# Kernel optimization log

Measured on AMD Instinct MI355X. Metric: run time of the kernel, lower is better.

Reference implementation:

```python
import jax, jax.numpy as jnp
import numpy as np

DIM = 768
HEADS = 12
HEAD_DIM = DIM // HEADS
ROPE_BASE = 100.0  # Dust3R uses freq=100 for its rotary embedding


def apply_rope(x):
    # x: [B, H, N, D] -> rotary embedding over token index (rotate-half form)
    B, H, N, D = x.shape
    pos = jnp.arange(N, dtype=jnp.float32)
    inv_freq = 1.0 / (ROPE_BASE ** (jnp.arange(0, D, 2, dtype=jnp.float32) / D))
    ang = pos[:, None] * inv_freq[None, :]            # [N, D/2]
    cos = jnp.concatenate([jnp.cos(ang), jnp.cos(ang)], axis=-1).astype(x.dtype)  # [N, D]
    sin = jnp.concatenate([jnp.sin(ang), jnp.sin(ang)], axis=-1).astype(x.dtype)
    x1, x2 = jnp.split(x, 2, axis=-1)
    x_rot = jnp.concatenate([-x2, x1], axis=-1)
    return x * cos + x_rot * sin


def setup_inputs() -> dict:
    key = jax.random.key(0)
    ks = jax.random.split(key, 8)
    B, N = 8, 1024
    scale = 0.02
    return {
        "query": jax.random.normal(ks[0], (B, N, DIM), jnp.float32),
        "key": jax.random.normal(ks[1], (B, N, DIM), jnp.float32),
        "value": jax.random.normal(ks[2], (B, N, DIM), jnp.float32),
        "Wq": jax.random.normal(ks[3], (DIM, DIM), jnp.float32) * scale,
        "Wk": jax.random.normal(ks[4], (DIM, DIM), jnp.float32) * scale,
        "Wv": jax.random.normal(ks[5], (DIM, DIM), jnp.float32) * scale,
        "Wo": jax.random.normal(ks[6], (DIM, DIM), jnp.float32) * scale,
        "bo": jax.random.normal(ks[7], (DIM,), jnp.float32) * scale,
    }


def reference(query, key, value, Wq, Wk, Wv, Wo, bo):
    B, Nq, C = query.shape
    H, D = HEADS, HEAD_DIM
    sm_scale = D ** -0.5
    # Linear projections (torch Linear: x @ W.T), split heads -> [B, H, N, D]
    q = jnp.einsum('bnc,dc->bnd', query, Wq).reshape(B, Nq, H, D).transpose(0, 2, 1, 3)
    k = jnp.einsum('bnc,dc->bnd', key, Wk).reshape(B, -1, H, D).transpose(0, 2, 1, 3)
    v = jnp.einsum('bnc,dc->bnd', value, Wv).reshape(B, -1, H, D).transpose(0, 2, 1, 3)
    q = apply_rope(q)
    k = apply_rope(k)
    attn = jnp.einsum('bhqd,bhkd->bhqk', q, k) * sm_scale
    attn = jax.nn.softmax(attn, axis=-1)
    x = jnp.einsum('bhqk,bhkd->bhqd', attn, v)
    x = x.transpose(0, 2, 1, 3).reshape(B, Nq, C)
    return jnp.einsum('bnc,dc->bnd', x, Wo) + bo
```

## Files before the change

kernel.cpp:

```cpp
#include <hip/hip_runtime.h>
#include <cmath>

typedef __bf16 bf16x8 __attribute__((ext_vector_type(8)));
typedef float f32x4 __attribute__((ext_vector_type(4)));
typedef unsigned short u16;

#define MFMA_BF16 __builtin_amdgcn_mfma_f32_16x16x32_bf16

__device__ __forceinline__ u16 f2bf(float f) {
  unsigned int u = __float_as_uint(f);
  u = (u + 0x7fffu + ((u >> 16) & 1u)) >> 16;
  return (u16)u;
}

__device__ __forceinline__ unsigned cvtpk(float lo, float hi) {
  unsigned r;
  asm("v_cvt_pk_bf16_f32 %0, %1, %2" : "=v"(r) : "v"(lo), "v"(hi));
  return r;
}

__device__ __forceinline__ void async16(const u16* g, u16* l) {
  __builtin_amdgcn_global_load_lds(
      (__attribute__((address_space(1))) void*)g,
      (__attribute__((address_space(3))) void*)l, 16, 0, 0);
}

__global__ __launch_bounds__(256) void cvt_bf16(const float4* __restrict__ in,
                                                uint2* __restrict__ out, int n4) {
  int i = blockIdx.x * 256 + threadIdx.x;
  if (i >= n4) return;
  float4 f = in[i];
  uint2 o;
  o.x = (unsigned)f2bf(f.x) | ((unsigned)f2bf(f.y) << 16);
  o.y = (unsigned)f2bf(f.z) | ((unsigned)f2bf(f.w) << 16);
  out[i] = o;
}

__global__ __launch_bounds__(256) void cvt_all(
    const float4* s0, const float4* s1, const float4* s2, const float4* s3,
    const float4* s4, const float4* s5, const float4* s6,
    uint2* d0, uint2* d1, uint2* d2, uint2* d3, uint2* d4, uint2* d5, uint2* d6) {
  int i = blockIdx.x * 256 + threadIdx.x;
  const float4* src;
  uint2* dst;
  int off;
  if (i < 1572864)      { src = s0; dst = d0; off = i; }
  else if (i < 3145728) { src = s1; dst = d1; off = i - 1572864; }
  else if (i < 4718592) { src = s2; dst = d2; off = i - 3145728; }
  else {
    int j = i - 4718592;
    int w = j / 147456;
    off = j - w * 147456;
    src = (w == 0) ? s3 : (w == 1) ? s4 : (w == 2) ? s5 : s6;
    dst = (w == 0) ? d3 : (w == 1) ? d4 : (w == 2) ? d5 : d6;
  }
  float4 f = src[off];
  uint2 o;
  o.x = (unsigned)f2bf(f.x) | ((unsigned)f2bf(f.y) << 16);
  o.y = (unsigned)f2bf(f.z) | ((unsigned)f2bf(f.w) << 16);
  dst[off] = o;
}

__device__ __forceinline__ void gemm_body(const u16* __restrict__ Ag,
                                          const u16* __restrict__ Wg,
                                          void* __restrict__ OutP,
                                          const float* __restrict__ bias,
                                          int mode, int bx, int by) {
  __shared__ alignas(16) u16 As[128][64];
  __shared__ alignas(16) u16 Bs[128][64];
  const int tid  = threadIdx.x;
  const int lane = tid & 63, wv = tid >> 6;
  const int l15  = lane & 15, quad = lane >> 4;
  const int row0 = bx * 128, col0 = by * 128;
  const int wr = (wv >> 1) * 64, wc = (wv & 1) * 64;
  const int swA = l15 & 7;

  size_t aSrc[4], bSrc[4];
  int dsts[4];
#pragma unroll
  for (int rr = 0; rr < 4; ++rr) {
    int c = rr * 256 + tid;
    int row = c >> 3, cp = c & 7;
    int gc = cp ^ (row & 7);
    aSrc[rr] = (size_t)(row0 + row) * 768 + gc * 8;
    bSrc[rr] = (size_t)(col0 + row) * 768 + gc * 8;
    dsts[rr] = c * 8;
  }

  f32x4 acc[4][4];
#pragma unroll
  for (int i = 0; i < 4; ++i)
#pragma unroll
    for (int j = 0; j < 4; ++j) acc[i][j] = (f32x4){0.f, 0.f, 0.f, 0.f};

  for (int kb = 0; kb < 768; kb += 64) {
#pragma unroll
    for (int rr = 0; rr < 4; ++rr) {
      async16(&Ag[aSrc[rr] + kb], &((u16*)As)[dsts[rr]]);
      async16(&Wg[bSrc[rr] + kb], &((u16*)Bs)[dsts[rr]]);
    }
    __syncthreads();
#pragma unroll
    for (int kd = 0; kd < 2; ++kd) {
      int cpk = ((kd * 4 + quad) ^ swA) * 8;
      bf16x8 af[4], bfr[4];
#pragma unroll
      for (int mt = 0; mt < 4; ++mt) af[mt] = *(const bf16x8*)&As[wr + mt * 16 + l15][cpk];
#pragma unroll
      for (int nt = 0; nt < 4; ++nt) bfr[nt] = *(const bf16x8*)&Bs[wc + nt * 16 + l15][cpk];
#pragma unroll
      for (int mt = 0; mt < 4; ++mt)
#pragma unroll
        for (int nt = 0; nt < 4; ++nt)
          acc[mt][nt] = MFMA_BF16(af[mt], bfr[nt], acc[mt][nt], 0, 0, 0);
    }
    __syncthreads();
  }

  if (mode == 3) {
    float* O = (float*)OutP;
#pragma unroll
    for (int mt = 0; mt < 4; ++mt)
#pragma unroll
      for (int r = 0; r < 4; ++r) {
        int m = row0 + wr + mt * 16 + quad * 4 + r;
#pragma unroll
        for (int nt = 0; nt < 4; ++nt) {
          int c = col0 + wc + nt * 16 + l15;
          O[(size_t)m * 768 + c] = acc[mt][nt][r] + bias[c];
        }
      }
  } else if (mode == 2) {
    u16* O = (u16*)OutP;
#pragma unroll
    for (int mt = 0; mt < 4; ++mt)
#pragma unroll
      for (int r = 0; r < 4; ++r) {
        int m = row0 + wr + mt * 16 + quad * 4 + r;
        int b = m >> 10, n = m & 1023;
#pragma unroll
        for (int nt = 0; nt < 4; ++nt) {
          int c = col0 + wc + nt * 16 + l15;
          O[(size_t)(b * 768 + c) * 1024 + n] = f2bf(acc[mt][nt][r]);
        }
      }
  } else {
    u16* O = (u16*)OutP;
    const float scale = (mode == 0) ? 0.125f * 1.44269504088896f : 1.0f;
    const float invf0 = exp2f(-6.6438561897747395f * (float)l15 * (1.0f / 32.0f));
    const float invf1 = exp2f(-6.6438561897747395f * (float)(16 + l15) * (1.0f / 32.0f));
#pragma unroll
    for (int mt = 0; mt < 4; ++mt)
#pragma unroll
      for (int r = 0; r < 4; ++r) {
        int m = row0 + wr + mt * 16 + quad * 4 + r;
        int b = m >> 10, n = m & 1023;
        float fn = (float)n;
        size_t rowbase = (size_t)b * 786432 + (size_t)n * 64;
#pragma unroll
        for (int nt = 0; nt < 2; ++nt) {
          float sv, cv;
          __sincosf(fn * (nt ? invf1 : invf0), &sv, &cv);
          float x1 = acc[mt][nt][r], x2 = acc[mt][nt + 2][r];
          int c1 = col0 + wc + nt * 16 + l15;
          int c2 = c1 + 32;
          O[rowbase + (size_t)(c1 >> 6) * 65536 + (c1 & 63)] = f2bf((x1 * cv - x2 * sv) * scale);
          O[rowbase + (size_t)(c2 >> 6) * 65536 + (c2 & 63)] = f2bf((x2 * cv + x1 * sv) * scale);
        }
      }
  }
}

__global__ __launch_bounds__(256, 3) void gemm768(const u16* __restrict__ A,
                                                  const u16* __restrict__ W,
                                                  void* __restrict__ OutP,
                                                  const float* __restrict__ bias,
                                                  int mode) {
  gemm_body(A, W, OutP, bias, mode, blockIdx.x, blockIdx.y);
}

__global__ __launch_bounds__(256, 3) void gemm_qkv(
    const u16* __restrict__ xq, const u16* __restrict__ xk, const u16* __restrict__ xv,
    const u16* __restrict__ wq, const u16* __restrict__ wk, const u16* __restrict__ wv,
    u16* __restrict__ qb, u16* __restrict__ kb, u16* __restrict__ vtb) {
  int z = blockIdx.z;
  const u16* A = (z == 0) ? xq : (z == 1) ? xk : xv;
  const u16* W = (z == 0) ? wq : (z == 1) ? wk : wv;
  void* O      = (z == 0) ? (void*)qb : (z == 1) ? (void*)kb : (void*)vtb;
  gemm_body(A, W, O, nullptr, z, blockIdx.x, blockIdx.y);
}

__global__ __launch_bounds__(256, 3) void attn_fused(const u16* __restrict__ Q,
                                                     const u16* __restrict__ K,
                                                     const u16* __restrict__ Vt,
                                                     u16* __restrict__ X) {
  __shared__ alignas(16) u16 KsF[2][4096];
  __shared__ alignas(16) u16 VsF[2][4096];
  __shared__ alignas(16) u16 Ps[4][2048];

  const int tid  = threadIdx.x;
  const int lane = tid & 63, wv = tid >> 6;
  const int l15  = lane & 15, quad = lane >> 4;
  const int bh = blockIdx.x, qt = blockIdx.y;
  const size_t base = (size_t)bh * 65536;
  const int sw8 = (quad ^ ((l15 >> 1) & 3)) * 8;
  const int swP = l15 & 7;

  const u16* Qg = Q + base + (size_t)qt * 8192;
  const u16* Kb = K + base;
  const u16* Vb = Vt + base;

  int kOff[2], vOff[2], dOff[2];
#pragma unroll
  for (int rr = 0; rr < 2; ++rr) {
    int c = rr * 256 + tid;
    int sub = c >> 8, rowi = (c >> 2) & 63, colc = c & 3;
    int cs = (colc ^ ((rowi >> 1) & 3)) * 8;
    kOff[rr] = rowi * 64 + sub * 32 + cs;
    vOff[rr] = rowi * 1024 + sub * 32 + cs;
    dOff[rr] = c * 8;
  }

  auto stageKV = [&](int kt, int bf) {
#pragma unroll
    for (int rr = 0; rr < 2; ++rr) {
      async16(&Kb[(size_t)kt * 64 + kOff[rr]], &KsF[bf][dOff[rr]]);
      async16(&Vb[(size_t)kt + vOff[rr]], &VsF[bf][dOff[rr]]);
    }
  };

  u16* Pflat = &Ps[0][0];
#pragma unroll
  for (int rr = 0; rr < 4; ++rr) {
    int c = rr * 256 + tid;
    async16(&Qg[c * 8], &Pflat[c * 8]);
  }
  stageKV(0, 0);
  __syncthreads();

  bf16x8 qf[2][2];
#pragma unroll
  for (int mt = 0; mt < 2; ++mt)
#pragma unroll
    for (int kd = 0; kd < 2; ++kd)
      qf[mt][kd] = *(const bf16x8*)&Pflat[(wv * 32 + mt * 16 + l15) * 64 + kd * 32 + quad * 8];
  __syncthreads();

  f32x4 o[2][4];
  float lsum[2] = {0.f, 0.f};
#pragma unroll
  for (int mt = 0; mt < 2; ++mt)
#pragma unroll
    for (int nt = 0; nt < 4; ++nt) o[mt][nt] = (f32x4){0.f, 0.f, 0.f, 0.f};

  u16* Pw = &Ps[wv][0];

  auto tile = [&](int t, int rb) {
    if (t < 15) stageKV((t + 1) * 64, rb ^ 1);

    f32x4 s[2][4];
#pragma unroll
    for (int ct = 0; ct < 4; ++ct) {
      bf16x8 kf0 = *(const bf16x8*)&KsF[rb][(ct * 16 + l15) * 32 + sw8];
      bf16x8 kf1 = *(const bf16x8*)&KsF[rb][2048 + (ct * 16 + l15) * 32 + sw8];
#pragma unroll
      for (int mt = 0; mt < 2; ++mt) {
        f32x4 tacc = (f32x4){0.f, 0.f, 0.f, 0.f};
        tacc = MFMA_BF16(kf0, qf[mt][0], tacc, 0, 0, 0);
        tacc = MFMA_BF16(kf1, qf[mt][1], tacc, 0, 0, 0);
        s[mt][ct] = tacc;
      }
    }

#pragma unroll
    for (int mt = 0; mt < 2; ++mt) {
#pragma unroll
      for (int ct = 0; ct < 4; ++ct) {
        float p0 = __builtin_amdgcn_exp2f(s[mt][ct][0]);
        float p1 = __builtin_amdgcn_exp2f(s[mt][ct][1]);
        float p2 = __builtin_amdgcn_exp2f(s[mt][ct][2]);
        float p3 = __builtin_amdgcn_exp2f(s[mt][ct][3]);
        lsum[mt] += (p0 + p1) + (p2 + p3);
        uint2 w;
        w.x = cvtpk(p0, p1);
        w.y = cvtpk(p2, p3);
        int c16 = 2 * ct + (quad >> 1);
        *(uint2*)&Pw[mt * 1024 + l15 * 64 + ((c16 ^ swP) << 3) + ((quad & 1) << 2)] = w;
      }
    }

#pragma unroll
    for (int ks = 0; ks < 2; ++ks) {
      int pc = ((ks * 4 + quad) ^ swP) << 3;
      bf16x8 pf0 = *(const bf16x8*)&Pw[l15 * 64 + pc];
      bf16x8 pf1 = *(const bf16x8*)&Pw[1024 + l15 * 64 + pc];
#pragma unroll
      for (int nt = 0; nt < 4; ++nt) {
        bf16x8 vf = *(const bf16x8*)&VsF[rb][ks * 2048 + (nt * 16 + l15) * 32 + sw8];
        o[0][nt] = MFMA_BF16(vf, pf0, o[0][nt], 0, 0, 0);
        o[1][nt] = MFMA_BF16(vf, pf1, o[1][nt], 0, 0, 0);
      }
    }
    __syncthreads();
  };

  for (int t = 0; t < 16; t += 2) {
    tile(t, 0);
    tile(t + 1, 1);
  }

  const int b = bh / 12, h = bh % 12;
#pragma unroll
  for (int mt = 0; mt < 2; ++mt) {
    float l = lsum[mt];
    l += __shfl_xor(l, 16);
    l += __shfl_xor(l, 32);
    float inv = __builtin_amdgcn_rcpf(l);
    int n = qt * 128 + wv * 32 + mt * 16 + l15;
    size_t rowoff = ((size_t)(b * 1024 + n)) * 768 + h * 64 + quad * 4;
#pragma unroll
    for (int nt = 0; nt < 4; ++nt) {
      uint2 w;
      w.x = cvtpk(o[mt][nt][0] * inv, o[mt][nt][1] * inv);
      w.y = cvtpk(o[mt][nt][2] * inv, o[mt][nt][3] * inv);
      *(uint2*)&X[rowoff + nt * 16] = w;
    }
  }
}

extern "C" void kernel_launch(void* const* d_in, const int* in_sizes, int n_in,
                              void* d_out, int out_size, void* d_ws, size_t ws_size,
                              hipStream_t stream) {
  const float* qin = (const float*)d_in[0];
  const float* kin = (const float*)d_in[1];
  const float* vin = (const float*)d_in[2];
  const float* Wq  = (const float*)d_in[3];
  const float* Wk  = (const float*)d_in[4];
  const float* Wv  = (const float*)d_in[5];
  const float* Wo  = (const float*)d_in[6];
  const float* bo  = (const float*)d_in[7];
  char* ws = (char*)d_ws;

  if (ws_size >= 80216064) {
    u16* xq16 = (u16*)(ws + 0);
    u16* xk16 = (u16*)(ws + 12582912);
    u16* xv16 = (u16*)(ws + 25165824);
    u16* qb   = (u16*)(ws + 37748736);
    u16* kb   = (u16*)(ws + 50331648);
    u16* vtb  = (u16*)(ws + 62914560);
    u16* wq16 = (u16*)(ws + 75497472);
    u16* wk16 = wq16 + 589824;
    u16* wv16 = wk16 + 589824;
    u16* wo16 = wv16 + 589824;
    u16* X    = xq16;

    cvt_all<<<20736, 256, 0, stream>>>(
        (const float4*)qin, (const float4*)kin, (const float4*)vin,
        (const float4*)Wq, (const float4*)Wk, (const float4*)Wv, (const float4*)Wo,
        (uint2*)xq16, (uint2*)xk16, (uint2*)xv16,
        (uint2*)wq16, (uint2*)wk16, (uint2*)wv16, (uint2*)wo16);
    gemm_qkv<<<dim3(64, 6, 3), 256, 0, stream>>>(xq16, xk16, xv16, wq16, wk16, wv16,
                                                 qb, kb, vtb);
    attn_fused<<<dim3(96, 8), 256, 0, stream>>>(qb, kb, vtb, X);
    gemm768<<<dim3(64, 6), 256, 0, stream>>>(X, wo16, d_out, bo, 3);
  } else {
    u16* xbuf = (u16*)(ws + 0);
    u16* qb   = (u16*)(ws + 12582912);
    u16* kb   = (u16*)(ws + 25165824);
    u16* vtb  = (u16*)(ws + 37748736);
    u16* wq16 = (u16*)(ws + 50331648);
    u16* wk16 = wq16 + 589824;
    u16* wv16 = wk16 + 589824;
    u16* wo16 = wv16 + 589824;

    cvt_bf16<<<576, 256, 0, stream>>>((const float4*)Wq, (uint2*)wq16, 147456);
    cvt_bf16<<<576, 256, 0, stream>>>((const float4*)Wk, (uint2*)wk16, 147456);
    cvt_bf16<<<576, 256, 0, stream>>>((const float4*)Wv, (uint2*)wv16, 147456);
    cvt_bf16<<<576, 256, 0, stream>>>((const float4*)Wo, (uint2*)wo16, 147456);

    dim3 ggrid(64, 6);
    cvt_bf16<<<6144, 256, 0, stream>>>((const float4*)qin, (uint2*)xbuf, 1572864);
    gemm768<<<ggrid, 256, 0, stream>>>(xbuf, wq16, (void*)qb, nullptr, 0);
    cvt_bf16<<<6144, 256, 0, stream>>>((const float4*)kin, (uint2*)xbuf, 1572864);
    gemm768<<<ggrid, 256, 0, stream>>>(xbuf, wk16, (void*)kb, nullptr, 1);
    cvt_bf16<<<6144, 256, 0, stream>>>((const float4*)vin, (uint2*)xbuf, 1572864);
    gemm768<<<ggrid, 256, 0, stream>>>(xbuf, wv16, (void*)vtb, nullptr, 2);

    attn_fused<<<dim3(96, 8), 256, 0, stream>>>(qb, kb, vtb, xbuf);

    gemm768<<<ggrid, 256, 0, stream>>>(xbuf, wo16, d_out, bo, 3);
  }
}
```

Measured before the change: 227.5 us.

## Feed softmax probabilities directly from registers into 16x16x16 MFMA for PV

Removes the per-wave shared-memory round trip for the probability tile. The S accumulator layout is reused directly as the B operand of the 16x16x16 bf16 MFMA, and the V fragments are read in matching 4-element slices. The Q staging buffer now aliases the K buffer, which frees the Ps LDS region and may allow higher occupancy. In exchange, the PV product needs twice as many smaller MFMA instructions, and the bf16 conversion moves from the packed cvt instruction to software rounding, which adds ALU work.

```diff
diff --git a/kernel.cpp b/kernel.cpp
--- a/kernel.cpp
+++ b/kernel.cpp
@@ -2,10 +2,27 @@
 #include <cmath>
 
 typedef __bf16 bf16x8 __attribute__((ext_vector_type(8)));
+typedef __bf16 bf16x4 __attribute__((ext_vector_type(4)));
+typedef short s16x4 __attribute__((ext_vector_type(4)));
 typedef float f32x4 __attribute__((ext_vector_type(4)));
 typedef unsigned short u16;
 
 #define MFMA_BF16 __builtin_amdgcn_mfma_f32_16x16x32_bf16
+
+__device__ __forceinline__ f32x4 mfma16(uint2 a, uint2 b, f32x4 c) {
+#if __has_builtin(__builtin_amdgcn_mfma_f32_16x16x16bf16_1k)
+  return __builtin_amdgcn_mfma_f32_16x16x16bf16_1k(
+      __builtin_bit_cast(s16x4, a), __builtin_bit_cast(s16x4, b), c, 0, 0, 0);
+#elif __has_builtin(__builtin_amdgcn_mfma_f32_16x16x16_bf16)
+  return __builtin_amdgcn_mfma_f32_16x16x16_bf16(
+      __builtin_bit_cast(bf16x4, a), __builtin_bit_cast(bf16x4, b), c, 0, 0, 0);
+#else
+  f32x4 d;
+  asm volatile("v_mfma_f32_16x16x16_bf16 %0, %1, %2, %3"
+               : "=v"(d) : "v"(a), "v"(b), "0"(c));
+  return d;
+#endif
+}
 
 __device__ __forceinline__ u16 f2bf(float f) {
   unsigned int u = __float_as_uint(f);
@@ -196,7 +213,6 @@
                                                      u16* __restrict__ X) {
   __shared__ alignas(16) u16 KsF[2][4096];
   __shared__ alignas(16) u16 VsF[2][4096];
-  __shared__ alignas(16) u16 Ps[4][2048];
 
   const int tid  = threadIdx.x;
   const int lane = tid & 63, wv = tid >> 6;
@@ -204,7 +220,7 @@
   const int bh = blockIdx.x, qt = blockIdx.y;
   const size_t base = (size_t)bh * 65536;
   const int sw8 = (quad ^ ((l15 >> 1) & 3)) * 8;
-  const int swP = l15 & 7;
+  const int g3  = (l15 >> 1) & 3;
 
   const u16* Qg = Q + base + (size_t)qt * 8192;
   const u16* Kb = K + base;
@@ -229,31 +245,31 @@
     }
   };
 
-  u16* Pflat = &Ps[0][0];
+  u16* Qs = &KsF[0][0];
 #pragma unroll
   for (int rr = 0; rr < 4; ++rr) {
     int c = rr * 256 + tid;
-    async16(&Qg[c * 8], &Pflat[c * 8]);
-  }
+    async16(&Qg[c * 8], &Qs[c * 8]);
+  }
+  __syncthreads();
+
+  bf16x8 qf[2][2];
+#pragma unroll
+  for (int mt = 0; mt < 2; ++mt)
+#pragma unroll
+    for (int kd = 0; kd < 2; ++kd)
+      qf[mt][kd] = *(const bf16x8*)&Qs[(wv * 32 + mt * 16 + l15) * 64 + kd * 32 + quad * 8];
+  __syncthreads();
+
   stageKV(0, 0);
   __syncthreads();
 
-  bf16x8 qf[2][2];
-#pragma unroll
-  for (int mt = 0; mt < 2; ++mt)
-#pragma unroll
-    for (int kd = 0; kd < 2; ++kd)
-      qf[mt][kd] = *(const bf16x8*)&Pflat[(wv * 32 + mt * 16 + l15) * 64 + kd * 32 + quad * 8];
-  __syncthreads();
-
   f32x4 o[2][4];
   float lsum[2] = {0.f, 0.f};
 #pragma unroll
   for (int mt = 0; mt < 2; ++mt)
 #pragma unroll
     for (int nt = 0; nt < 4; ++nt) o[mt][nt] = (f32x4){0.f, 0.f, 0.f, 0.f};
-
-  u16* Pw = &Ps[wv][0];
 
   auto tile = [&](int t, int rb) {
     if (t < 15) stageKV((t + 1) * 64, rb ^ 1);
@@ -273,32 +289,25 @@
     }
 
 #pragma unroll
-    for (int mt = 0; mt < 2; ++mt) {
-#pragma unroll
-      for (int ct = 0; ct < 4; ++ct) {
+    for (int ct = 0; ct < 4; ++ct) {
+      int voff = (ct >> 1) * 2048 + (((2 * (ct & 1) + (quad >> 1)) ^ g3) << 3) +
+                 ((quad & 1) << 2);
+      uint2 vfw[4];
+#pragma unroll
+      for (int nt = 0; nt < 4; ++nt)
+        vfw[nt] = *(const uint2*)&VsF[rb][voff + (nt * 16 + l15) * 32];
+#pragma unroll
+      for (int mt = 0; mt < 2; ++mt) {
         float p0 = __builtin_amdgcn_exp2f(s[mt][ct][0]);
         float p1 = __builtin_amdgcn_exp2f(s[mt][ct][1]);
         float p2 = __builtin_amdgcn_exp2f(s[mt][ct][2]);
         float p3 = __builtin_amdgcn_exp2f(s[mt][ct][3]);
         lsum[mt] += (p0 + p1) + (p2 + p3);
-        uint2 w;
-        w.x = cvtpk(p0, p1);
-        w.y = cvtpk(p2, p3);
-        int c16 = 2 * ct + (quad >> 1);
-        *(uint2*)&Pw[mt * 1024 + l15 * 64 + ((c16 ^ swP) << 3) + ((quad & 1) << 2)] = w;
-      }
-    }
-
-#pragma unroll
-    for (int ks = 0; ks < 2; ++ks) {
-      int pc = ((ks * 4 + quad) ^ swP) << 3;
-      bf16x8 pf0 = *(const bf16x8*)&Pw[l15 * 64 + pc];
-      bf16x8 pf1 = *(const bf16x8*)&Pw[1024 + l15 * 64 + pc];
-#pragma unroll
-      for (int nt = 0; nt < 4; ++nt) {
-        bf16x8 vf = *(const bf16x8*)&VsF[rb][ks * 2048 + (nt * 16 + l15) * 32 + sw8];
-        o[0][nt] = MFMA_BF16(vf, pf0, o[0][nt], 0, 0, 0);
-        o[1][nt] = MFMA_BF16(vf, pf1, o[1][nt], 0, 0, 0);
+        uint2 pw;
+        pw.x = (unsigned)f2bf(p0) | ((unsigned)f2bf(p1) << 16);
+        pw.y = (unsigned)f2bf(p2) | ((unsigned)f2bf(p3) << 16);
+#pragma unroll
+        for (int nt = 0; nt < 4; ++nt) o[mt][nt] = mfma16(vfw[nt], pw, o[mt][nt]);
       }
     }
     __syncthreads();
```

Result: no change. 229.4 us (+0.9%).
